# Performance work log

Hardware: AMD Instinct MI355X
Metric: run time of the kernel (lower is better)

Reference implementation:

```python
import jax, jax.numpy as jnp
import numpy as np

N, E, F_IN, NCLS, H = 50000, 800000, 128, 10, 64


def setup_inputs() -> dict:
    key = jax.random.key(0)
    ks = jax.random.split(key, 24)
    p = lambda k, shp: (jax.random.normal(k, shp, dtype=jnp.float32) * 0.1)
    inp = {
        'x': jax.random.normal(ks[0], (N, F_IN), dtype=jnp.float32),
        'edge_index': jax.random.randint(ks[1], (2, E), 0, N, dtype=jnp.int64),
        'gcn1_W': p(ks[2], (F_IN, 128)), 'gcn1_b': p(ks[3], (128,)),
        'gcn2_W': p(ks[4], (128, 64)),  'gcn2_b': p(ks[5], (64,)),
        'gcn3_W': p(ks[6], (64, 32)),   'gcn3_b': p(ks[7], (32,)),
        'gat_W': p(ks[8], (32, 32)), 'gat_a_src': p(ks[9], (32,)),
        'gat_a_dst': p(ks[10], (32,)), 'gat_b': p(ks[11], (32,)),
        'lstm_Wih_f': p(ks[12], (4 * H, 32)), 'lstm_bih_f': p(ks[13], (4 * H,)), 'lstm_bhh_f': p(ks[14], (4 * H,)),
        'lstm_Wih_b': p(ks[15], (4 * H, 32)), 'lstm_bih_b': p(ks[16], (4 * H,)), 'lstm_bhh_b': p(ks[17], (4 * H,)),
        'bn_gamma': jnp.ones((2 * H,), jnp.float32), 'bn_beta': jnp.zeros((2 * H,), jnp.float32),
        'fc_W': p(ks[18], (NCLS, 2 * H)), 'fc_b': p(ks[19], (NCLS,)),
    }
    return inp


def _forward(x, edge_index, gcn1_W, gcn1_b, gcn2_W, gcn2_b, gcn3_W, gcn3_b,
             gat_W, gat_a_src, gat_a_dst, gat_b,
             lstm_Wih_f, lstm_bih_f, lstm_bhh_f, lstm_Wih_b, lstm_bih_b, lstm_bhh_b,
             bn_gamma, bn_beta, fc_W, fc_b):
    n = x.shape[0]
    loop = jnp.arange(n)
    row = jnp.concatenate([edge_index[0], loop])  # source nodes (+ self loops)
    col = jnp.concatenate([edge_index[1], loop])  # target nodes
    deg = jax.ops.segment_sum(jnp.ones_like(col, dtype=x.dtype), col, num_segments=n)
    dis = jax.lax.rsqrt(jnp.maximum(deg, 1e-12))  # deg >= 1 due to self loops
    norm = dis[row] * dis[col]

    def gcn(h, W, b):
        h = h @ W
        return jax.ops.segment_sum(h[row] * norm[:, None], col, num_segments=n) + b

    h = jax.nn.relu(gcn(x, gcn1_W, gcn1_b))
    h = jax.nn.relu(gcn(h, gcn2_W, gcn2_b))
    h = gcn(h, gcn3_W, gcn3_b)

    # GAT (1 head), self loops already in row/col, softmax over incoming edges per target
    g = h @ gat_W
    e = jax.nn.leaky_relu((g @ gat_a_src)[row] + (g @ gat_a_dst)[col], negative_slope=0.2)
    m = jax.ops.segment_max(e, col, num_segments=n)
    ee = jnp.exp(e - m[col])
    att = ee / jax.ops.segment_sum(ee, col, num_segments=n)[col]
    h = jax.ops.segment_sum(g[row] * att[:, None], col, num_segments=n) + gat_b
    h = jax.nn.relu(h)

    # bidirectional LSTM with seq_len=1, h0=c0=0 -> single cell step per direction
    def lstm_dir(xx, Wih, bih, bhh):
        gt = xx @ Wih.T + bih + bhh
        i, f, c, o = jnp.split(gt, 4, axis=-1)  # torch gate order i,f,g,o
        return jax.nn.sigmoid(o) * jnp.tanh(jax.nn.sigmoid(i) * jnp.tanh(c))

    r = jnp.concatenate([lstm_dir(h, lstm_Wih_f, lstm_bih_f, lstm_bhh_f),
                         lstm_dir(h, lstm_Wih_b, lstm_bih_b, lstm_bhh_b)], axis=-1)
    # eval mode: dropout = identity; BatchNorm1d with running_mean=0, running_var=1
    r = r * (bn_gamma / jnp.sqrt(jnp.float32(1.0 + 1e-5))) + bn_beta
    return r @ fc_W.T + fc_b


def reference(x, edge_index, gcn1_W, gcn1_b, gcn2_W, gcn2_b, gcn3_W, gcn3_b,
              gat_W, gat_a_src, gat_a_dst, gat_b,
              lstm_Wih_f, lstm_bih_f, lstm_bhh_f, lstm_Wih_b, lstm_bih_b, lstm_bhh_b,
              bn_gamma, bn_beta, fc_W, fc_b):
    return _forward(x, edge_index, gcn1_W, gcn1_b, gcn2_W, gcn2_b, gcn3_W, gcn3_b,
                    gat_W, gat_a_src, gat_a_dst, gat_b,
                    lstm_Wih_f, lstm_bih_f, lstm_bhh_f, lstm_Wih_b, lstm_bih_b, lstm_bhh_b,
                    bn_gamma, bn_beta, fc_W, fc_b)
```

## Files before the change

kernel.cpp:

```cpp
#include <hip/hip_runtime.h>
#include <hip/hip_bf16.h>
#include <math.h>

typedef __hip_bfloat16 bf16;

#define NN 50000
#define EE 800000
#define EPB 4096
#define NBK 196
#define BCAP 6144

__device__ __forceinline__ float b2f(bf16 v) { return __bfloat162float(v); }
__device__ __forceinline__ float rcp_(float x) { return __builtin_amdgcn_rcpf(x); }
__device__ __forceinline__ float sigmoidf_(float x) { return rcp_(1.0f + __expf(-x)); }
__device__ __forceinline__ float tanhf_(float x) {
    float xx = fminf(fmaxf(x, -15.0f), 15.0f);
    float e = __expf(2.0f * xx);
    return (e - 1.0f) * rcp_(e + 1.0f);
}
__device__ __forceinline__ float leakyf_(float x) { return x > 0.0f ? x : 0.2f * x; }
__device__ __forceinline__ unsigned short f2bf(float f) {
    unsigned u = __float_as_uint(f);
    unsigned r = (u + 0x7FFFu + ((u >> 16) & 1u)) >> 16;
    return (unsigned short)r;
}
__device__ __forceinline__ unsigned pack2(float a, float b) {
    return (unsigned)f2bf(a) | ((unsigned)f2bf(b) << 16);
}
__device__ __forceinline__ float lo_(unsigned u) { return __uint_as_float(u << 16); }
__device__ __forceinline__ float hi_(unsigned u) { return __uint_as_float(u & 0xFFFF0000u); }

#define OFF_W1 0
#define OFF_B1 16384
#define OFF_W2 16512
#define OFF_B2 24704
#define OFF_W3 24768
#define OFF_B3 26816
#define OFF_GATW 26848
#define OFF_GAS 27872
#define OFF_GAD 27904
#define OFF_GAB 27936
#define OFF_WIHF 27968
#define OFF_BIHF 36160
#define OFF_BHHF 36416
#define OFF_WIHB 36672
#define OFF_BIHB 44864
#define OFF_BHHB 45120
#define OFF_GAMMA 45376
#define OFF_BETA 45504
#define OFF_FCW 45632
#define OFF_FCB 46912
#define WTOTAL 46922

struct WSrc { const void* p[20]; };

__global__ void k_detect(const unsigned short* __restrict__ xraw,
                         const unsigned int* __restrict__ eraw, int* __restrict__ flags) {
    __shared__ int f32f, i64f;
    int t = threadIdx.x;
    if (t == 0) { f32f = 0; i64f = 1; }
    __syncthreads();
    for (int i = t; i < 4096; i += 256) {
        unsigned short u = xraw[i];
        int ex = (u >> 7) & 0xFF;
        if (ex >= 0xC0) atomicOr(&f32f, 1);
        if (eraw[2 * i + 1] != 0u) atomicAnd(&i64f, 0);
    }
    __syncthreads();
    if (t == 0) { flags[0] = f32f; flags[1] = i64f; }
}

__global__ void k_cvt_w(WSrc srcs, float* __restrict__ dst, const int* __restrict__ flags,
                        int total) {
    constexpr int WOFF[21] = {OFF_W1,   OFF_B1,   OFF_W2,   OFF_B2,   OFF_W3,   OFF_B3,
                              OFF_GATW, OFF_GAS,  OFF_GAD,  OFF_GAB,  OFF_WIHF, OFF_BIHF,
                              OFF_BHHF, OFF_WIHB, OFF_BIHB, OFF_BHHB, OFF_GAMMA, OFF_BETA,
                              OFF_FCW,  OFF_FCB,  WTOTAL};
    int i = blockIdx.x * 256 + threadIdx.x;
    if (i >= total) return;
    int tn = 0;
#pragma unroll
    for (int j = 1; j < 20; ++j)
        if (i >= WOFF[j]) tn = j;
    int local = i - WOFF[tn];
    if (flags[0]) dst[i] = ((const float*)srcs.p[tn])[local];
    else dst[i] = b2f(((const bf16*)srcs.p[tn])[local]);
}

__global__ __launch_bounds__(256) void k_hist(const void* __restrict__ eraw,
                                              unsigned* __restrict__ gh,
                                              const int* __restrict__ flags) {
    __shared__ int h[256];
    int t = threadIdx.x, b = blockIdx.x;
    h[t] = 0;
    __syncthreads();
    int e0 = b * EPB;
    bool i64 = flags[1] != 0;
    for (int i = t; i < EPB; i += 256) {
        int e = e0 + i;
        if (e < EE) {
            int d = i64 ? (int)((const long long*)eraw)[EE + e] : ((const int*)eraw)[EE + e];
            d = min(max(d, 0), NN - 1);
            atomicAdd(&h[d >> 8], 1);
        }
    }
    __syncthreads();
    gh[b * 256 + t] = (unsigned)h[t];
}

__global__ __launch_bounds__(256) void k_bscan(const unsigned* __restrict__ gh,
                                               unsigned* __restrict__ gh2,
                                               int* __restrict__ bb, int* __restrict__ rptr) {
    __shared__ int s[256];
    int t = threadIdx.x;
    unsigned run = 0;
    for (int blk = 0; blk < NBK; ++blk) {
        unsigned v = gh[blk * 256 + t];
        gh2[blk * 256 + t] = run;
        run += v;
    }
    s[t] = (int)run;
    __syncthreads();
    for (int o = 1; o < 256; o <<= 1) {
        int x = (t >= o) ? s[t - o] : 0;
        __syncthreads();
        s[t] += x;
        __syncthreads();
    }
    bb[t] = s[t] - (int)run;
    if (t == 0) rptr[NN] = EE;
}

__global__ __launch_bounds__(256) void k_scatter(const void* __restrict__ eraw,
                                                 const unsigned* __restrict__ gh2,
                                                 const int* __restrict__ bb,
                                                 int2* __restrict__ ebkt,
                                                 const int* __restrict__ flags) {
    __shared__ unsigned cur[256];
    int t = threadIdx.x, b = blockIdx.x;
    cur[t] = gh2[b * 256 + t] + (unsigned)bb[t];
    __syncthreads();
    int e0 = b * EPB;
    bool i64 = flags[1] != 0;
    for (int i = t; i < EPB; i += 256) {
        int e = e0 + i;
        if (e < EE) {
            int sn, d;
            if (i64) {
                sn = (int)((const long long*)eraw)[e];
                d = (int)((const long long*)eraw)[EE + e];
            } else {
                sn = ((const int*)eraw)[e];
                d = ((const int*)eraw)[EE + e];
            }
            sn = min(max(sn, 0), NN - 1);
            d = min(max(d, 0), NN - 1);
            unsigned pos = atomicAdd(&cur[d >> 8], 1u);
            if (pos < (unsigned)EE) ebkt[pos] = make_int2(sn, d);
        }
    }
}

__global__ __launch_bounds__(256) void k_bucket_csr(const int2* __restrict__ ebkt,
                                                    const int* __restrict__ bb,
                                                    int* __restrict__ rptr,
                                                    float* __restrict__ dis,
                                                    int* __restrict__ csr_src) {
    __shared__ int hist[256];
    __shared__ int excl[256];
    __shared__ int cur[256];
    __shared__ int sorted[BCAP];
    int t = threadIdx.x, b = blockIdx.x;
    int s0 = bb[b], s1 = bb[b + 1];
    int len = min(s1 - s0, BCAP);
    hist[t] = 0;
    __syncthreads();
    for (int i = t; i < len; i += 256) atomicAdd(&hist[ebkt[s0 + i].y & 255], 1);
    __syncthreads();
    int v = hist[t];
    excl[t] = v;
    __syncthreads();
    for (int o = 1; o < 256; o <<= 1) {
        int x = (t >= o) ? excl[t - o] : 0;
        __syncthreads();
        excl[t] += x;
        __syncthreads();
    }
    int loc = excl[t] - v;
    int node = b * 256 + t;
    if (node < NN) {
        rptr[node] = s0 + loc;
        dis[node] = rsqrtf((float)(v + 1));
    }
    cur[t] = loc;
    __syncthreads();
    for (int i = t; i < len; i += 256) {
        int2 p = ebkt[s0 + i];
        int pos = atomicAdd(&cur[p.y & 255], 1);
        if (pos < BCAP) sorted[pos] = p.x;
    }
    __syncthreads();
    for (int i = t; i < len; i += 256) csr_src[s0 + i] = sorted[i];
}

template <int KIN, int KOUT, int MODE, bool SCALE>
__global__ __launch_bounds__(256) void k_tile_mm(const void* __restrict__ A,
                                                 const float* __restrict__ W,
                                                 unsigned* __restrict__ C, int n,
                                                 const int* __restrict__ flags, int want,
                                                 const float* __restrict__ dis) {
    if (want >= 0 && flags[0] != want) return;
    constexpr int BK = 32;
    constexpr int AST = BK + 4;
    constexpr int CPT = KOUT / 16;
    __shared__ float As[64 * AST];
    __shared__ float Ws[BK * KOUT];
    int t = threadIdx.x;
    int jc = t & 15;
    int ng = t >> 4;
    int base = blockIdx.x * 64;
    float acc[4][CPT];
#pragma unroll
    for (int i = 0; i < 4; ++i)
#pragma unroll
        for (int c = 0; c < CPT; ++c) acc[i][c] = 0.f;
    int snode = t >> 2;
    int gnode = min(base + snode, n - 1);
    int koff = (t & 3) * 8;
    for (int k0 = 0; k0 < KIN; k0 += BK) {
        {
            const float4* src = (const float4*)(W + k0 * KOUT);
            float4* dst = (float4*)Ws;
#pragma unroll
            for (int p = 0; p < BK * KOUT / 1024; ++p) dst[t + p * 256] = src[t + p * 256];
        }
        if (MODE == 0) {
            const unsigned* xr = (const unsigned*)A + (size_t)gnode * (KIN / 2) + (k0 + koff) / 2;
            unsigned u0 = xr[0], u1 = xr[1], u2 = xr[2], u3 = xr[3];
            float* d = As + snode * AST + koff;
            d[0] = lo_(u0); d[1] = hi_(u0);
            d[2] = lo_(u1); d[3] = hi_(u1);
            d[4] = lo_(u2); d[5] = hi_(u2);
            d[6] = lo_(u3); d[7] = hi_(u3);
        } else {
            const float4* ar = (const float4*)((const float*)A + (size_t)gnode * KIN + k0 + koff);
            float4 v0 = ar[0], v1 = ar[1];
            float4* d = (float4*)(As + snode * AST + koff);
            d[0] = v0;
            d[1] = v1;
        }
        __syncthreads();
#pragma unroll 8
        for (int k = 0; k < BK; ++k) {
            float w[CPT];
            const float* wr = Ws + k * KOUT + jc * CPT;
            if constexpr (CPT >= 4) {
#pragma unroll
                for (int c = 0; c < CPT; c += 4) {
                    float4 wv = *(const float4*)(wr + c);
                    w[c] = wv.x; w[c + 1] = wv.y; w[c + 2] = wv.z; w[c + 3] = wv.w;
                }
            } else {
                float2 wv = *(const float2*)wr;
                w[0] = wv.x; w[1] = wv.y;
            }
            float a0 = As[(ng * 4 + 0) * AST + k];
            float a1 = As[(ng * 4 + 1) * AST + k];
            float a2 = As[(ng * 4 + 2) * AST + k];
            float a3 = As[(ng * 4 + 3) * AST + k];
#pragma unroll
            for (int c = 0; c < CPT; ++c) {
                acc[0][c] += a0 * w[c];
                acc[1][c] += a1 * w[c];
                acc[2][c] += a2 * w[c];
                acc[3][c] += a3 * w[c];
            }
        }
        __syncthreads();
    }
#pragma unroll
    for (int i = 0; i < 4; ++i) {
        int node = base + ng * 4 + i;
        if (node < n) {
            float sc = SCALE ? dis[node] : 1.0f;
            unsigned* cr = C + (size_t)node * (KOUT / 2) + jc * (CPT / 2);
#pragma unroll
            for (int c = 0; c < CPT; c += 2)
                cr[c / 2] = pack2(acc[i][c] * sc, acc[i][c + 1] * sc);
        }
    }
}

template <bool RELU>
__global__ void k_agg128(const unsigned* __restrict__ t, const int* __restrict__ rptr,
                         const int* __restrict__ csr_src, const float* __restrict__ dis,
                         const float* __restrict__ bias, float* __restrict__ out, int n) {
    int wave = (blockIdx.x * blockDim.x + threadIdx.x) >> 6;
    int lane = threadIdx.x & 63;
    if (wave >= n) return;
    int dst = wave;
    float dd = dis[dst];
    float ax, ay;
    {
        unsigned u = t[(size_t)dst * 64 + lane];
        ax = lo_(u);
        ay = hi_(u);
    }
    int s = __builtin_amdgcn_readfirstlane(max(0, min(rptr[dst], EE)));
    int e = __builtin_amdgcn_readfirstlane(max(s, min(rptr[dst + 1], EE)));
    int j = s;
    for (; j + 8 <= e; j += 8) {
        int i0 = csr_src[j], i1 = csr_src[j + 1], i2 = csr_src[j + 2], i3 = csr_src[j + 3];
        int i4 = csr_src[j + 4], i5 = csr_src[j + 5], i6 = csr_src[j + 6], i7 = csr_src[j + 7];
        unsigned u0 = t[(size_t)i0 * 64 + lane], u1 = t[(size_t)i1 * 64 + lane];
        unsigned u2 = t[(size_t)i2 * 64 + lane], u3 = t[(size_t)i3 * 64 + lane];
        unsigned u4 = t[(size_t)i4 * 64 + lane], u5 = t[(size_t)i5 * 64 + lane];
        unsigned u6 = t[(size_t)i6 * 64 + lane], u7 = t[(size_t)i7 * 64 + lane];
        ax += (lo_(u0) + lo_(u1)) + (lo_(u2) + lo_(u3)) + (lo_(u4) + lo_(u5)) + (lo_(u6) + lo_(u7));
        ay += (hi_(u0) + hi_(u1)) + (hi_(u2) + hi_(u3)) + (hi_(u4) + hi_(u5)) + (hi_(u6) + hi_(u7));
    }
    for (; j + 4 <= e; j += 4) {
        int i0 = csr_src[j], i1 = csr_src[j + 1], i2 = csr_src[j + 2], i3 = csr_src[j + 3];
        unsigned u0 = t[(size_t)i0 * 64 + lane], u1 = t[(size_t)i1 * 64 + lane];
        unsigned u2 = t[(size_t)i2 * 64 + lane], u3 = t[(size_t)i3 * 64 + lane];
        ax += (lo_(u0) + lo_(u1)) + (lo_(u2) + lo_(u3));
        ay += (hi_(u0) + hi_(u1)) + (hi_(u2) + hi_(u3));
    }
    for (; j < e; ++j) {
        unsigned u0 = t[(size_t)csr_src[j] * 64 + lane];
        ax += lo_(u0);
        ay += hi_(u0);
    }
    float2 bv = *(const float2*)(bias + 2 * lane);
    float vx = ax * dd + bv.x;
    float vy = ay * dd + bv.y;
    if (RELU) { vx = fmaxf(vx, 0.f); vy = fmaxf(vy, 0.f); }
    *(float2*)(out + (size_t)dst * 128 + 2 * lane) = make_float2(vx, vy);
}

template <bool RELU>
__global__ void k_agg64(const unsigned* __restrict__ t, const int* __restrict__ rptr,
                        const int* __restrict__ csr_src, const float* __restrict__ dis,
                        const float* __restrict__ bias, float* __restrict__ out, int n) {
    int wave = (blockIdx.x * blockDim.x + threadIdx.x) >> 6;
    int lane = threadIdx.x & 63;
    if (wave >= n) return;
    int dst = wave;
    int half = lane >> 5, l32 = lane & 31;
    float dd = dis[dst];
    float ax = 0.f, ay = 0.f;
    if (!half) {
        unsigned u = t[(size_t)dst * 32 + l32];
        ax = lo_(u);
        ay = hi_(u);
    }
    int s = max(0, min(rptr[dst], EE));
    int e = max(s, min(rptr[dst + 1], EE));
    int cnt = e - s;
    int pairs = cnt >> 1;
    int p = 0;
    for (; p + 4 <= pairs; p += 4) {
        int jb = s + 2 * p + half;
        int i0 = csr_src[jb], i1 = csr_src[jb + 2], i2 = csr_src[jb + 4], i3 = csr_src[jb + 6];
        unsigned u0 = t[(size_t)i0 * 32 + l32], u1 = t[(size_t)i1 * 32 + l32];
        unsigned u2 = t[(size_t)i2 * 32 + l32], u3 = t[(size_t)i3 * 32 + l32];
        ax += (lo_(u0) + lo_(u1)) + (lo_(u2) + lo_(u3));
        ay += (hi_(u0) + hi_(u1)) + (hi_(u2) + hi_(u3));
    }
    for (; p < pairs; ++p) {
        int i0 = csr_src[s + 2 * p + half];
        unsigned u0 = t[(size_t)i0 * 32 + l32];
        ax += lo_(u0);
        ay += hi_(u0);
    }
    if ((cnt & 1) && !half) {
        unsigned u0 = t[(size_t)csr_src[e - 1] * 32 + l32];
        ax += lo_(u0);
        ay += hi_(u0);
    }
    ax += __shfl_down(ax, 32);
    ay += __shfl_down(ay, 32);
    if (!half) {
        float2 bv = *(const float2*)(bias + 2 * l32);
        float vx = ax * dd + bv.x;
        float vy = ay * dd + bv.y;
        if (RELU) { vx = fmaxf(vx, 0.f); vy = fmaxf(vy, 0.f); }
        *(float2*)(out + (size_t)dst * 64 + 2 * l32) = make_float2(vx, vy);
    }
}

template <bool RELU>
__global__ void k_agg32(const unsigned* __restrict__ t, const int* __restrict__ rptr,
                        const int* __restrict__ csr_src, const float* __restrict__ dis,
                        const float* __restrict__ bias, float* __restrict__ out, int n) {
    int wave = (blockIdx.x * blockDim.x + threadIdx.x) >> 6;
    int lane = threadIdx.x & 63;
    if (wave >= n) return;
    int dst = wave;
    int q = lane >> 4, l16 = lane & 15;
    float dd = dis[dst];
    float ax = 0.f, ay = 0.f;
    if (q == 0) {
        unsigned u = t[(size_t)dst * 16 + l16];
        ax = lo_(u);
        ay = hi_(u);
    }
    int s = max(0, min(rptr[dst], EE));
    int e = max(s, min(rptr[dst + 1], EE));
    int cnt = e - s;
    int quads = cnt >> 2;
    int p = 0;
    for (; p + 4 <= quads; p += 4) {
        int jb = s + 4 * p + q;
        int i0 = csr_src[jb], i1 = csr_src[jb + 4], i2 = csr_src[jb + 8], i3 = csr_src[jb + 12];
        unsigned u0 = t[(size_t)i0 * 16 + l16], u1 = t[(size_t)i1 * 16 + l16];
        unsigned u2 = t[(size_t)i2 * 16 + l16], u3 = t[(size_t)i3 * 16 + l16];
        ax += (lo_(u0) + lo_(u1)) + (lo_(u2) + lo_(u3));
        ay += (hi_(u0) + hi_(u1)) + (hi_(u2) + hi_(u3));
    }
    for (; p < quads; ++p) {
        int i0 = csr_src[s + 4 * p + q];
        unsigned u0 = t[(size_t)i0 * 16 + l16];
        ax += lo_(u0);
        ay += hi_(u0);
    }
    int rem = cnt - 4 * quads;
    if (q < rem) {
        unsigned u0 = t[(size_t)csr_src[s + 4 * quads + q] * 16 + l16];
        ax += lo_(u0);
        ay += hi_(u0);
    }
    ax += __shfl_down(ax, 32);
    ay += __shfl_down(ay, 32);
    ax += __shfl_down(ax, 16);
    ay += __shfl_down(ay, 16);
    if (q == 0) {
        float2 bv = *(const float2*)(bias + 2 * l16);
        float vx = ax * dd + bv.x;
        float vy = ay * dd + bv.y;
        if (RELU) { vx = fmaxf(vx, 0.f); vy = fmaxf(vy, 0.f); }
        *(float2*)(out + (size_t)dst * 32 + 2 * l16) = make_float2(vx, vy);
    }
}

__global__ void k_gat_vec(const unsigned* __restrict__ g, const float* __restrict__ a_src,
                          const float* __restrict__ a_dst, float* __restrict__ asrc,
                          float* __restrict__ adst, int n) {
    int i = blockIdx.x * 256 + threadIdx.x;
    if (i >= n) return;
    float s = 0.0f, d = 0.0f;
    const unsigned* gr = g + (size_t)i * 16;
#pragma unroll
    for (int k = 0; k < 16; ++k) {
        unsigned u = gr[k];
        float v0 = lo_(u), v1 = hi_(u);
        s += v0 * a_src[2 * k] + v1 * a_src[2 * k + 1];
        d += v0 * a_dst[2 * k] + v1 * a_dst[2 * k + 1];
    }
    asrc[i] = s;
    adst[i] = d;
}

__global__ void k_gat_agg(const unsigned* __restrict__ g, const int* __restrict__ rptr,
                          const int* __restrict__ csr_src, const float* __restrict__ asrc,
                          const float* __restrict__ adst, const float* __restrict__ gat_b,
                          float* __restrict__ out, int n) {
    int wave = (blockIdx.x * blockDim.x + threadIdx.x) >> 6;
    int lane = threadIdx.x & 63;
    if (wave >= n) return;
    int dst = wave;
    int q = lane >> 4, l16 = lane & 15;
    float ad = adst[dst];
    int s = max(0, min(rptr[dst], EE));
    int e = max(s, min(rptr[dst + 1], EE));
    float ax = 0.f, ay = 0.f, denom = 0.f;
    if (q == 0) {
        float w0 = __expf(fminf(leakyf_(asrc[dst] + ad), 80.f));
        unsigned u = g[(size_t)dst * 16 + l16];
        ax = lo_(u) * w0;
        ay = hi_(u) * w0;
        denom = w0;
    }
    int cnt = e - s;
    int quads = cnt >> 2;
    int p = 0;
    for (; p + 4 <= quads; p += 4) {
        int jb = s + 4 * p + q;
        int i0 = csr_src[jb], i1 = csr_src[jb + 4], i2 = csr_src[jb + 8], i3 = csr_src[jb + 12];
        float a0 = asrc[i0], a1 = asrc[i1], a2 = asrc[i2], a3 = asrc[i3];
        unsigned u0 = g[(size_t)i0 * 16 + l16], u1 = g[(size_t)i1 * 16 + l16];
        unsigned u2 = g[(size_t)i2 * 16 + l16], u3 = g[(size_t)i3 * 16 + l16];
        float w0 = __expf(fminf(leakyf_(a0 + ad), 80.f));
        float w1 = __expf(fminf(leakyf_(a1 + ad), 80.f));
        float w2 = __expf(fminf(leakyf_(a2 + ad), 80.f));
        float w3 = __expf(fminf(leakyf_(a3 + ad), 80.f));
        denom += (w0 + w1) + (w2 + w3);
        ax += lo_(u0) * w0 + lo_(u1) * w1 + lo_(u2) * w2 + lo_(u3) * w3;
        ay += hi_(u0) * w0 + hi_(u1) * w1 + hi_(u2) * w2 + hi_(u3) * w3;
    }
    for (; p < quads; ++p) {
        int i0 = csr_src[s + 4 * p + q];
        float wgt = __expf(fminf(leakyf_(asrc[i0] + ad), 80.f));
        unsigned u0 = g[(size_t)i0 * 16 + l16];
        denom += wgt;
        ax += lo_(u0) * wgt;
        ay += hi_(u0) * wgt;
    }
    int rem = cnt - 4 * quads;
    if (q < rem) {
        int i0 = csr_src[s + 4 * quads + q];
        float wgt = __expf(fminf(leakyf_(asrc[i0] + ad), 80.f));
        unsigned u0 = g[(size_t)i0 * 16 + l16];
        denom += wgt;
        ax += lo_(u0) * wgt;
        ay += hi_(u0) * wgt;
    }
    ax += __shfl_down(ax, 32);
    ay += __shfl_down(ay, 32);
    denom += __shfl_down(denom, 32);
    ax += __shfl_down(ax, 16);
    ay += __shfl_down(ay, 16);
    denom += __shfl_down(denom, 16);
    if (q == 0) {
        float r = rcp_(denom);
        float vx = fmaxf(ax * r + gat_b[2 * l16], 0.f);
        float vy = fmaxf(ay * r + gat_b[2 * l16 + 1], 0.f);
        *(float2*)(out + (size_t)dst * 32 + 2 * l16) = make_float2(vx, vy);
    }
}

__global__ __launch_bounds__(256, 3) void k_lstm_fc(const float* __restrict__ h,
                                                    const float* __restrict__ wp,
                                                    void* __restrict__ out,
                                                    const int* __restrict__ flags, int n) {
    __shared__ float hs[64 * 32];
    __shared__ float rs[64 * 129];
    __shared__ float ps[4 * 640];
    int t = threadIdx.x;
    int base = blockIdx.x * 64;

    for (int i = t; i < 512; i += 256) {
        int nd = i >> 3, k4 = i & 7;
        int node = min(base + nd, n - 1);
        ((float4*)hs)[i] = ((const float4*)h)[(size_t)node * 8 + k4];
    }

    int row = t & 127;
    int grp = t >> 7;
    int dir = row >> 6, j = row & 63;
    const float* W = wp + (dir ? OFF_WIHB : OFF_WIHF);
    const float* bi = wp + (dir ? OFF_BIHB : OFF_BIHF);
    const float* bh = wp + (dir ? OFF_BHHB : OFF_BHHF);

    float w_i[32], w_c[32], w_o[32];
    {
        const float4* wip = (const float4*)(W + (size_t)j * 32);
        const float4* wcp = (const float4*)(W + (size_t)(128 + j) * 32);
        const float4* wop = (const float4*)(W + (size_t)(192 + j) * 32);
#pragma unroll
        for (int k4 = 0; k4 < 8; ++k4) {
            float4 a = wip[k4], b = wcp[k4], c = wop[k4];
            w_i[4 * k4 + 0] = a.x; w_i[4 * k4 + 1] = a.y; w_i[4 * k4 + 2] = a.z; w_i[4 * k4 + 3] = a.w;
            w_c[4 * k4 + 0] = b.x; w_c[4 * k4 + 1] = b.y; w_c[4 * k4 + 2] = b.z; w_c[4 * k4 + 3] = b.w;
            w_o[4 * k4 + 0] = c.x; w_o[4 * k4 + 1] = c.y; w_o[4 * k4 + 2] = c.z; w_o[4 * k4 + 3] = c.w;
        }
    }
    float bI = bi[j] + bh[j];
    float bC = bi[128 + j] + bh[128 + j];
    float bO = bi[192 + j] + bh[192 + j];
    float gsc = wp[OFF_GAMMA + row] * rsqrtf(1.0f + 1e-5f);
    float gbe = wp[OFF_BETA + row];

    __syncthreads();

    int slot0 = grp * 32;
    for (int nn = 0; nn < 32; ++nn) {
        const float* hvp = hs + (slot0 + nn) * 32;
        float ai = bI, ac = bC, ao = bO;
#pragma unroll
        for (int k = 0; k < 32; ++k) {
            float hk = hvp[k];
            ai += hk * w_i[k];
            ac += hk * w_c[k];
            ao += hk * w_o[k];
        }
        float v = sigmoidf_(ao) * tanhf_(sigmoidf_(ai) * tanhf_(ac));
        rs[(slot0 + nn) * 129 + row] = v * gsc + gbe;
    }
    __syncthreads();

    {
        int nd = t & 63, quarter = t >> 6;
        const float* fcw = wp + OFF_FCW;
        int jbase = quarter * 32;
        float p10[10];
#pragma unroll
        for (int c = 0; c < 10; ++c) p10[c] = 0.f;
#pragma unroll 4
        for (int k = 0; k < 32; ++k) {
            float r = rs[nd * 129 + jbase + k];
#pragma unroll
            for (int c = 0; c < 10; ++c) p10[c] += r * fcw[c * 128 + jbase + k];
        }
#pragma unroll
        for (int c = 0; c < 10; ++c) ps[quarter * 640 + nd * 10 + c] = p10[c];
    }
    __syncthreads();
    bool f32o = flags[0] != 0;
    for (int idx = t; idx < 640; idx += 256) {
        int gnode = base + idx / 10;
        if (gnode < n) {
            int c = idx % 10;
            float v = wp[OFF_FCB + c] + ps[idx] + ps[640 + idx] + ps[1280 + idx] + ps[1920 + idx];
            if (f32o) ((float*)out)[(size_t)base * 10 + idx] = v;
            else ((unsigned short*)out)[(size_t)base * 10 + idx] = f2bf(v);
        }
    }
}

extern "C" void kernel_launch(void* const* d_in, const int* in_sizes, int n_in,
                              void* d_out, int out_size, void* d_ws, size_t ws_size,
                              hipStream_t stream) {
    const int N = NN;

    char* w = (char*)d_ws;
    auto alloc = [&](size_t bytes) {
        void* p = (void*)w;
        w += (bytes + 255) & ~(size_t)255;
        return p;
    };
    int* flags = (int*)alloc(256);
    float* wpool = (float*)alloc((size_t)WTOTAL * 4);
    float* dis = (float*)alloc((size_t)N * 4);
    int* rptr = (int*)alloc((size_t)(N + 1) * 4);
    int* csr_src = (int*)alloc((size_t)EE * 4);
    unsigned* gh = (unsigned*)alloc((size_t)NBK * 256 * 4);
    unsigned* gh2 = (unsigned*)alloc((size_t)NBK * 256 * 4);
    int* bb = (int*)alloc(1024);
    int2* ebkt = (int2*)alloc((size_t)EE * 8);
    float* asrc = (float*)alloc((size_t)N * 4);
    float* adst = (float*)alloc((size_t)N * 4);
    unsigned* bufT = (unsigned*)alloc((size_t)N * 64 * 4);
    float* bufH = (float*)alloc((size_t)N * 128 * 4);

    WSrc ws_srcs;
    for (int i = 0; i < 20; ++i) ws_srcs.p[i] = d_in[2 + i];

    const int NB = (N + 255) / 256;
    const int AGG = (N + 3) / 4;
    const int TMB = (N + 63) / 64;
    const int LFB = (N + 63) / 64;
    const int WB = (WTOTAL + 255) / 256;

    k_detect<<<1, 256, 0, stream>>>((const unsigned short*)d_in[0],
                                    (const unsigned int*)d_in[1], flags);
    k_cvt_w<<<WB, 256, 0, stream>>>(ws_srcs, wpool, flags, WTOTAL);
    k_hist<<<NBK, 256, 0, stream>>>(d_in[1], gh, flags);
    k_bscan<<<1, 256, 0, stream>>>(gh, gh2, bb, rptr);
    k_scatter<<<NBK, 256, 0, stream>>>(d_in[1], gh2, bb, ebkt, flags);
    k_bucket_csr<<<NBK, 256, 0, stream>>>(ebkt, bb, rptr, dis, csr_src);

    k_tile_mm<128, 128, 0, true><<<TMB, 256, 0, stream>>>(d_in[0], wpool + OFF_W1, bufT, N, flags, 0, dis);
    k_tile_mm<128, 128, 1, true><<<TMB, 256, 0, stream>>>(d_in[0], wpool + OFF_W1, bufT, N, flags, 1, dis);
    k_agg128<true><<<AGG, 256, 0, stream>>>(bufT, rptr, csr_src, dis, wpool + OFF_B1, bufH, N);
    k_tile_mm<128, 64, 1, true><<<TMB, 256, 0, stream>>>(bufH, wpool + OFF_W2, bufT, N, flags, -1, dis);
    k_agg64<true><<<AGG, 256, 0, stream>>>(bufT, rptr, csr_src, dis, wpool + OFF_B2, bufH, N);
    k_tile_mm<64, 32, 1, true><<<TMB, 256, 0, stream>>>(bufH, wpool + OFF_W3, bufT, N, flags, -1, dis);
    k_agg32<false><<<AGG, 256, 0, stream>>>(bufT, rptr, csr_src, dis, wpool + OFF_B3, bufH, N);
    k_tile_mm<32, 32, 1, false><<<TMB, 256, 0, stream>>>(bufH, wpool + OFF_GATW, bufT, N, flags, -1, dis);
    k_gat_vec<<<NB, 256, 0, stream>>>(bufT, wpool + OFF_GAS, wpool + OFF_GAD, asrc, adst, N);
    k_gat_agg<<<AGG, 256, 0, stream>>>(bufT, rptr, csr_src, asrc, adst, wpool + OFF_GAB, bufH, N);
    k_lstm_fc<<<LFB, 256, 0, stream>>>(bufH, wpool, d_out, flags, N);
}
```

Baseline: 375.6 us.

## Split LSTM+FC into register-tiled gate GEMM and separate FC kernel

Replaces the fused LSTM/FC kernel, where each thread held 96 weight registers and looped over nodes one at a time, with a register-tiled GEMM kernel. That kernel keeps a pre-transposed, gate-interleaved weight matrix in shared memory and computes 4 nodes x 12 gate columns per thread, one grid dimension per direction. A small prep kernel builds the transposed weights, fused biases and BN scale. The FC projection moves to its own kernel that reads the gate results from a new global buffer. This trades the register-pressure-limited fused kernel for extra global traffic (a 25.6MB intermediate written and read) and two extra launches.

New measurement: 377.0 us. Within noise of the previous version (+0.4%).

```diff
diff --git a/kernel.cpp b/kernel.cpp
--- a/kernel.cpp
+++ b/kernel.cpp
@@ -52,6 +52,12 @@
 #define OFF_FCB 46912
 #define WTOTAL 46922
 
+#define AX_WT 0
+#define AX_BT 12288
+#define AX_GSC 12672
+#define AX_GBE 12800
+#define AX_TOTAL 12928
+
 struct WSrc { const void* p[20]; };
 
 __global__ void k_detect(const unsigned short* __restrict__ xraw,
@@ -85,6 +91,25 @@
     int local = i - WOFF[tn];
     if (flags[0]) dst[i] = ((const float*)srcs.p[tn])[local];
     else dst[i] = b2f(((const bf16*)srcs.p[tn])[local]);
+}
+
+__global__ void k_prep(const float* __restrict__ wp, float* __restrict__ aux) {
+    int dir = blockIdx.x;
+    int t = threadIdx.x;
+    const float* W = wp + (dir ? OFF_WIHB : OFF_WIHF);
+    const float* bi = wp + (dir ? OFF_BIHB : OFF_BIHF);
+    const float* bh = wp + (dir ? OFF_BHHB : OFF_BHHF);
+    int col = t;
+    int j = col / 3, gate = col - 3 * j;
+    int srcrow = j + (gate == 1 ? 128 : (gate == 2 ? 192 : 0));
+    const float* src = W + (size_t)srcrow * 32;
+    for (int k = 0; k < 32; ++k) aux[AX_WT + dir * 6144 + k * 192 + col] = src[k];
+    aux[AX_BT + dir * 192 + col] = bi[srcrow] + bh[srcrow];
+    if (t < 64) {
+        int jj = dir * 64 + t;
+        aux[AX_GSC + jj] = wp[OFF_GAMMA + jj] * rsqrtf(1.0f + 1e-5f);
+        aux[AX_GBE + jj] = wp[OFF_BETA + jj];
+    }
 }
 
 __global__ __launch_bounds__(256) void k_hist(const void* __restrict__ eraw,
@@ -529,66 +554,101 @@
     }
 }
 
-__global__ __launch_bounds__(256, 3) void k_lstm_fc(const float* __restrict__ h,
-                                                    const float* __restrict__ wp,
-                                                    void* __restrict__ out,
-                                                    const int* __restrict__ flags, int n) {
-    __shared__ float hs[64 * 32];
+__global__ __launch_bounds__(256) void k_gates(const float* __restrict__ h,
+                                               const float* __restrict__ aux,
+                                               float* __restrict__ rbuf, int n) {
+    constexpr int AST = 36;
+    __shared__ float As[64 * AST];
+    __shared__ float Ws[32 * 192];
+    int t = threadIdx.x;
+    int dir = blockIdx.y;
+    int jc = t & 15;
+    int ng = t >> 4;
+    int base = blockIdx.x * 64;
+    {
+        const float4* src = (const float4*)(aux + AX_WT + dir * 6144);
+        float4* dst = (float4*)Ws;
+#pragma unroll
+        for (int p = 0; p < 6; ++p) dst[t + p * 256] = src[t + p * 256];
+    }
+    {
+        int snode = t >> 2;
+        int gnode = min(base + snode, n - 1);
+        int koff = (t & 3) * 8;
+        const float4* ar = (const float4*)(h + (size_t)gnode * 32 + koff);
+        float4* d = (float4*)(As + snode * AST + koff);
+        d[0] = ar[0];
+        d[1] = ar[1];
+    }
+    float acc[4][12];
+    {
+        const float4* bt = (const float4*)(aux + AX_BT + dir * 192 + jc * 12);
+        float4 b0 = bt[0], b1 = bt[1], b2 = bt[2];
+        float b12[12] = {b0.x, b0.y, b0.z, b0.w, b1.x, b1.y, b1.z, b1.w,
+                         b2.x, b2.y, b2.z, b2.w};
+#pragma unroll
+        for (int i = 0; i < 4; ++i)
+#pragma unroll
+            for (int c = 0; c < 12; ++c) acc[i][c] = b12[c];
+    }
+    __syncthreads();
+#pragma unroll 8
+    for (int k = 0; k < 32; ++k) {
+        float w[12];
+        const float* wr = Ws + k * 192 + jc * 12;
+#pragma unroll
+        for (int c = 0; c < 12; c += 4) {
+            float4 wv = *(const float4*)(wr + c);
+            w[c] = wv.x; w[c + 1] = wv.y; w[c + 2] = wv.z; w[c + 3] = wv.w;
+        }
+        float a0 = As[(ng * 4 + 0) * AST + k];
+        float a1 = As[(ng * 4 + 1) * AST + k];
+        float a2 = As[(ng * 4 + 2) * AST + k];
+        float a3 = As[(ng * 4 + 3) * AST + k];
+#pragma unroll
+        for (int c = 0; c < 12; ++c) {
+            acc[0][c] += a0 * w[c];
+            acc[1][c] += a1 * w[c];
+            acc[2][c] += a2 * w[c];
+            acc[3][c] += a3 * w[c];
+        }
+    }
+    float4 gscv = *(const float4*)(aux + AX_GSC + dir * 64 + jc * 4);
+    float4 gbev = *(const float4*)(aux + AX_GBE + dir * 64 + jc * 4);
+#pragma unroll
+    for (int i = 0; i < 4; ++i) {
+        int node = base + ng * 4 + i;
+        if (node < n) {
+            float v0 = sigmoidf_(acc[i][2]) * tanhf_(sigmoidf_(acc[i][0]) * tanhf_(acc[i][1]));
+            float v1 = sigmoidf_(acc[i][5]) * tanhf_(sigmoidf_(acc[i][3]) * tanhf_(acc[i][4]));
+            float v2 = sigmoidf_(acc[i][8]) * tanhf_(sigmoidf_(acc[i][6]) * tanhf_(acc[i][7]));
+            float v3 = sigmoidf_(acc[i][11]) * tanhf_(sigmoidf_(acc[i][9]) * tanhf_(acc[i][10]));
+            float4 rv;
+            rv.x = v0 * gscv.x + gbev.x;
+            rv.y = v1 * gscv.y + gbev.y;
+            rv.z = v2 * gscv.z + gbev.z;
+            rv.w = v3 * gscv.w + gbev.w;
+            *(float4*)(rbuf + (size_t)node * 128 + dir * 64 + jc * 4) = rv;
+        }
+    }
+}
+
+__global__ __launch_bounds__(256) void k_fc(const float* __restrict__ rbuf,
+                                            const float* __restrict__ wp,
+                                            void* __restrict__ out,
+                                            const int* __restrict__ flags, int n) {
     __shared__ float rs[64 * 129];
     __shared__ float ps[4 * 640];
     int t = threadIdx.x;
     int base = blockIdx.x * 64;
-
-    for (int i = t; i < 512; i += 256) {
-        int nd = i >> 3, k4 = i & 7;
+    for (int i = t; i < 2048; i += 256) {
+        int nd = i >> 5, k4 = i & 31;
         int node = min(base + nd, n - 1);
-        ((float4*)hs)[i] = ((const float4*)h)[(size_t)node * 8 + k4];
-    }
-
-    int row = t & 127;
-    int grp = t >> 7;
-    int dir = row >> 6, j = row & 63;
-    const float* W = wp + (dir ? OFF_WIHB : OFF_WIHF);
-    const float* bi = wp + (dir ? OFF_BIHB : OFF_BIHF);
-    const float* bh = wp + (dir ? OFF_BHHB : OFF_BHHF);
-
-    float w_i[32], w_c[32], w_o[32];
-    {
-        const float4* wip = (const float4*)(W + (size_t)j * 32);
-        const float4* wcp = (const float4*)(W + (size_t)(128 + j) * 32);
-        const float4* wop = (const float4*)(W + (size_t)(192 + j) * 32);
-#pragma unroll
-        for (int k4 = 0; k4 < 8; ++k4) {
-            float4 a = wip[k4], b = wcp[k4], c = wop[k4];
-            w_i[4 * k4 + 0] = a.x; w_i[4 * k4 + 1] = a.y; w_i[4 * k4 + 2] = a.z; w_i[4 * k4 + 3] = a.w;
-            w_c[4 * k4 + 0] = b.x; w_c[4 * k4 + 1] = b.y; w_c[4 * k4 + 2] = b.z; w_c[4 * k4 + 3] = b.w;
-            w_o[4 * k4 + 0] = c.x; w_o[4 * k4 + 1] = c.y; w_o[4 * k4 + 2] = c.z; w_o[4 * k4 + 3] = c.w;
-        }
-    }
-    float bI = bi[j] + bh[j];
-    float bC = bi[128 + j] + bh[128 + j];
-    float bO = bi[192 + j] + bh[192 + j];
-    float gsc = wp[OFF_GAMMA + row] * rsqrtf(1.0f + 1e-5f);
-    float gbe = wp[OFF_BETA + row];
-
-    __syncthreads();
-
-    int slot0 = grp * 32;
-    for (int nn = 0; nn < 32; ++nn) {
-        const float* hvp = hs + (slot0 + nn) * 32;
-        float ai = bI, ac = bC, ao = bO;
-#pragma unroll
-        for (int k = 0; k < 32; ++k) {
-            float hk = hvp[k];
-            ai += hk * w_i[k];
-            ac += hk * w_c[k];
-            ao += hk * w_o[k];
-        }
-        float v = sigmoidf_(ao) * tanhf_(sigmoidf_(ai) * tanhf_(ac));
-        rs[(slot0 + nn) * 129 + row] = v * gsc + gbe;
-    }
-    __syncthreads();
-
+        float4 v = ((const float4*)rbuf)[(size_t)node * 32 + k4];
+        float* d = rs + nd * 129 + k4 * 4;
+        d[0] = v.x; d[1] = v.y; d[2] = v.z; d[3] = v.w;
+    }
+    __syncthreads();
     {
         int nd = t & 63, quarter = t >> 6;
         const float* fcw = wp + OFF_FCW;
@@ -631,6 +691,7 @@
     };
     int* flags = (int*)alloc(256);
     float* wpool = (float*)alloc((size_t)WTOTAL * 4);
+    float* aux = (float*)alloc((size_t)AX_TOTAL * 4);
     float* dis = (float*)alloc((size_t)N * 4);
     int* rptr = (int*)alloc((size_t)(N + 1) * 4);
     int* csr_src = (int*)alloc((size_t)EE * 4);
@@ -642,6 +703,7 @@
     float* adst = (float*)alloc((size_t)N * 4);
     unsigned* bufT = (unsigned*)alloc((size_t)N * 64 * 4);
     float* bufH = (float*)alloc((size_t)N * 128 * 4);
+    float* rbuf = (float*)alloc((size_t)N * 128 * 4);
 
     WSrc ws_srcs;
     for (int i = 0; i < 20; ++i) ws_srcs.p[i] = d_in[2 + i];
@@ -649,12 +711,12 @@
     const int NB = (N + 255) / 256;
     const int AGG = (N + 3) / 4;
     const int TMB = (N + 63) / 64;
-    const int LFB = (N + 63) / 64;
     const int WB = (WTOTAL + 255) / 256;
 
     k_detect<<<1, 256, 0, stream>>>((const unsigned short*)d_in[0],
                                     (const unsigned int*)d_in[1], flags);
     k_cvt_w<<<WB, 256, 0, stream>>>(ws_srcs, wpool, flags, WTOTAL);
+    k_prep<<<2, 192, 0, stream>>>(wpool, aux);
     k_hist<<<NBK, 256, 0, stream>>>(d_in[1], gh, flags);
     k_bscan<<<1, 256, 0, stream>>>(gh, gh2, bb, rptr);
     k_scatter<<<NBK, 256, 0, stream>>>(d_in[1], gh2, bb, ebkt, flags);
@@ -670,5 +732,6 @@
     k_tile_mm<32, 32, 1, false><<<TMB, 256, 0, stream>>>(bufH, wpool + OFF_GATW, bufT, N, flags, -1, dis);
     k_gat_vec<<<NB, 256, 0, stream>>>(bufT, wpool + OFF_GAS, wpool + OFF_GAD, asrc, adst, N);
     k_gat_agg<<<AGG, 256, 0, stream>>>(bufT, rptr, csr_src, asrc, adst, wpool + OFF_GAB, bufH, N);
-    k_lstm_fc<<<LFB, 256, 0, stream>>>(bufH, wpool, d_out, flags, N);
-}
+    k_gates<<<dim3(TMB, 2), 256, 0, stream>>>(bufH, aux, rbuf, N);
+    k_fc<<<TMB, 256, 0, stream>>>(rbuf, wpool, d_out, flags, N);
+}
```
